# Optimization experiments

Measured on AMD Instinct MI355X. Metric: run time of the kernel, lower is better.

The kernel has to match this reference:

```python
import jax, jax.numpy as jnp
import numpy as np

TEMPERATURE = 0.2
EPS = 1e-12  # F.normalize clamp eps


def setup_inputs() -> dict:
    key = jax.random.key(0)
    k1, k2 = jax.random.split(key)
    N, D = 4096, 256
    Z_1 = jax.random.normal(k1, (N, D), dtype=jnp.float32)
    Z_2 = jax.random.normal(k2, (N, D), dtype=jnp.float32)
    return {"Z_1": Z_1, "Z_2": Z_2}


def reference(Z_1, Z_2):
    N = Z_1.shape[0]
    M = 2 * N
    # concat views and L2-normalize rows (torch F.normalize semantics)
    Z = jnp.concatenate([Z_1, Z_2], axis=0)  # [2N, D]
    Z = Z / jnp.maximum(jnp.linalg.norm(Z, axis=1, keepdims=True), EPS)
    # full similarity matrix [2N, 2N]
    sim = jnp.matmul(Z, Z.T) / TEMPERATURE
    # positive for row i is column (i + N) mod 2N (other view of same sample,
    # identity diagonal discarded as in create_contrastive_masks)
    idx = jnp.arange(M)
    pos = sim[idx, (idx + N) % M]  # [2N]
    # logits = [pos, negatives]; label = 0 => CE = logsumexp(pos U negs) - pos.
    # pos U negs = all columns except the identity diagonal.
    diag = idx[:, None] == idx[None, :]
    sim_masked = jnp.where(diag, -jnp.inf, sim)
    lse = jax.nn.logsumexp(sim_masked, axis=1)  # [2N]
    return jnp.mean(lse - pos)
```

## Files before the change

kernel.cpp:

```cpp
#include <hip/hip_runtime.h>
#include <cstdint>
#include <cstddef>

#define TINV 5.0f
#define C5L2E 7.2134752044448170f
#define NROWS 4096
#define DDIM 256
#define MM 8192

typedef __bf16 bf16x8 __attribute__((ext_vector_type(8)));
typedef float f32x4 __attribute__((ext_vector_type(4)));

typedef const void __attribute__((address_space(1)))* gas_ptr;
typedef void __attribute__((address_space(3)))* las_ptr;

__global__ __launch_bounds__(256, 2)
void nrm_kernel(const float* __restrict__ Z1, const float* __restrict__ Z2,
                unsigned short* __restrict__ Zb, float* __restrict__ rowsumAcc) {
    if (blockIdx.x < 32) rowsumAcc[blockIdx.x * 256 + threadIdx.x] = 0.f;
    const int w = threadIdx.x >> 6, lane = threadIdx.x & 63;
    const int row = blockIdx.x * 4 + w;
    const float* src = row < NROWS ? Z1 + (size_t)row * DDIM
                                   : Z2 + (size_t)(row - NROWS) * DDIM;
    float4 v = reinterpret_cast<const float4*>(src)[lane];
    float ss = v.x*v.x + v.y*v.y + v.z*v.z + v.w*v.w;
    #pragma unroll
    for (int m = 1; m < 64; m <<= 1) ss += __shfl_xor(ss, m, 64);
    float inv = 1.0f / fmaxf(sqrtf(ss), 1e-12f);
    float o[4] = { v.x*inv, v.y*inv, v.z*inv, v.w*inv };
    unsigned short us[4];
    #pragma unroll
    for (int e = 0; e < 4; ++e) {
        unsigned int b = __builtin_bit_cast(unsigned int, o[e]);
        b += 0x7FFFu + ((b >> 16) & 1u);
        us[e] = (unsigned short)(b >> 16);
    }
    reinterpret_cast<ushort4*>(Zb + (size_t)row * DDIM)[lane] =
        *reinterpret_cast<ushort4*>(us);
}

__device__ __forceinline__ void stage32(const unsigned short* Zb, char* ldsdst,
                                        int rowStart, int tid) {
    const char* base = reinterpret_cast<const char*>(Zb) + (size_t)rowStart * 512;
    #pragma unroll
    for (int it = 0; it < 8; ++it) {
        int L = it * 4096 + tid * 16;
        int row = L >> 9;
        int soff = row * 512 + ((L & 511) ^ ((row & 15) << 4));
        __builtin_amdgcn_global_load_lds((gas_ptr)(base + soff), (las_ptr)(ldsdst + L),
                                         16, 0, 0);
    }
}

__global__ __launch_bounds__(256, 2)
void sim_lse_kernel(const unsigned short* __restrict__ Zb,
                    float* __restrict__ rowsumAcc,
                    float* __restrict__ posArr) {
    __shared__ char lds[65536];
    __shared__ float colRed[4][128];
    const int tid = threadIdx.x;
    const int lane = tid & 63;
    const int w = tid >> 6;
    const int r15 = lane & 15, hi = lane >> 4;
    const int r = blockIdx.x >> 3;
    const int s = blockIdx.x & 7;
    const int e0 = r & 7, e1 = e0 ^ 4;
    const int nt = 8 + ((s == e0) || (s == e1));
    const int extraHalf = (s == e1) ? 1 : 0;
    const int R0 = r * 128;

    int koff[8];
    #pragma unroll
    for (int kk = 0; kk < 8; ++kk)
        koff[kk] = ((hi << 4) | (kk << 6)) ^ (r15 << 4);

    stage32(Zb, lds, R0, tid);
    stage32(Zb, lds + 32768, R0 + 64, tid);
    __syncthreads();
    bf16x8 qf[2][8];
    {
        const char* ab = lds + ((w >> 1) << 15);
        #pragma unroll
        for (int mf = 0; mf < 2; ++mf)
            #pragma unroll
            for (int kk = 0; kk < 8; ++kk)
                qf[mf][kk] = *reinterpret_cast<const bf16x8*>(
                    ab + ((w & 1) * 32 + mf * 16 + r15) * 512 + koff[kk]);
    }
    __syncthreads();

    int baddr[8];
    #pragma unroll
    for (int kk = 0; kk < 8; ++kk) baddr[kk] = r15 * 512 + koff[kk];

    float rowsum[2][4] = {{0,0,0,0},{0,0,0,0}};
    const int iBase = R0 + w * 32 + (hi << 2);

    auto colOf = [&](int t) -> int {
        int d = (t < 8) ? (s + ((t >> 1) << 3)) : 32;
        int half = (t < 8) ? (t & 1) : extraHalf;
        return ((r + d) & 63) * 128 + half * 64;
    };

    stage32(Zb, lds, colOf(0), tid);

    for (int t = 0; t < nt; ++t) {
        const int C0 = colOf(t);
        const int cur = (t & 1) << 15;
        if (t < nt - 1) {
            stage32(Zb, lds + (cur ^ 32768), colOf(t + 1), tid);
            asm volatile("s_waitcnt vmcnt(8)" ::: "memory");
        } else {
            asm volatile("s_waitcnt vmcnt(0)" ::: "memory");
        }
        __builtin_amdgcn_s_barrier();
        __builtin_amdgcn_sched_barrier(0);

        const int mode = (t == 8) ? 2 : ((s == 0 && t < 2) ? 1 : 0);
        #pragma unroll
        for (int nf = 0; nf < 4; ++nf) {
            f32x4 acc0 = {0,0,0,0}, acc1 = {0,0,0,0};
            #pragma unroll
            for (int kk = 0; kk < 8; ++kk) {
                bf16x8 b = *reinterpret_cast<const bf16x8*>(lds + cur + nf * 8192 + baddr[kk]);
                acc0 = __builtin_amdgcn_mfma_f32_16x16x32_bf16(qf[0][kk], b, acc0, 0, 0, 0);
                acc1 = __builtin_amdgcn_mfma_f32_16x16x32_bf16(qf[1][kk], b, acc1, 0, 0, 0);
            }
            const int j = C0 + nf * 16 + r15;
            if (mode == 0) {
                float s8 = 0.f;
                #pragma unroll
                for (int mf = 0; mf < 2; ++mf) {
                    const f32x4 a = mf ? acc1 : acc0;
                    #pragma unroll
                    for (int rr = 0; rr < 4; ++rr) {
                        float e = __builtin_amdgcn_exp2f(fmaf(a[rr], C5L2E, -C5L2E));
                        rowsum[mf][rr] += e;
                        s8 += e;
                    }
                }
                s8 += __shfl_xor(s8, 16, 64);
                s8 += __shfl_xor(s8, 32, 64);
                if (hi == 0) colRed[w][(t & 1) * 64 + nf * 16 + r15] = s8;
            } else if (mode == 1) {
                #pragma unroll
                for (int mf = 0; mf < 2; ++mf) {
                    const f32x4 a = mf ? acc1 : acc0;
                    #pragma unroll
                    for (int rr = 0; rr < 4; ++rr) {
                        const int i = iBase + mf * 16 + rr;
                        if (j != i)
                            rowsum[mf][rr] += __builtin_amdgcn_exp2f(fmaf(a[rr], C5L2E, -C5L2E));
                    }
                }
            } else {
                #pragma unroll
                for (int mf = 0; mf < 2; ++mf) {
                    const f32x4 a = mf ? acc1 : acc0;
                    #pragma unroll
                    for (int rr = 0; rr < 4; ++rr) {
                        const int i = iBase + mf * 16 + rr;
                        rowsum[mf][rr] += __builtin_amdgcn_exp2f(fmaf(a[rr], C5L2E, -C5L2E));
                        if (j == (i ^ 4096)) posArr[i] = a[rr] * TINV;
                    }
                }
            }
        }
        asm volatile("" ::: "memory");
        __builtin_amdgcn_sched_barrier(0);
        __builtin_amdgcn_s_barrier();

        if ((t & 1) == 1 && !(s == 0 && t == 1)) {
            if (tid < 128) {
                float v = colRed[0][tid] + colRed[1][tid] + colRed[2][tid] + colRed[3][tid];
                const int cc = ((r + s + ((t >> 1) << 3)) & 63) * 128;
                atomicAdd(&rowsumAcc[cc + tid], v);
            }
        }
    }

    #pragma unroll
    for (int mf = 0; mf < 2; ++mf)
        #pragma unroll
        for (int rr = 0; rr < 4; ++rr) {
            float v = rowsum[mf][rr];
            v += __shfl_xor(v, 1, 64);
            v += __shfl_xor(v, 2, 64);
            v += __shfl_xor(v, 4, 64);
            v += __shfl_xor(v, 8, 64);
            if (r15 == 0) atomicAdd(&rowsumAcc[iBase + mf * 16 + rr], v);
        }
}

__global__ __launch_bounds__(128)
void fin1_kernel(const float* __restrict__ rowsumAcc, const float* __restrict__ posArr,
                 float* __restrict__ blockSums) {
    const int tid = threadIdx.x;
    const int i = blockIdx.x * 128 + tid;
    double v = (double)(logf(rowsumAcc[i]) + 5.0f - posArr[i]);
    #pragma unroll
    for (int m = 1; m < 64; m <<= 1) v += __shfl_xor(v, m, 64);
    __shared__ double red[2];
    if ((tid & 63) == 0) red[tid >> 6] = v;
    __syncthreads();
    if (tid == 0) blockSums[blockIdx.x] = (float)(red[0] + red[1]);
}

__global__ __launch_bounds__(64)
void fin2_kernel(const float* __restrict__ blockSums, float* __restrict__ out) {
    double v = (double)blockSums[threadIdx.x];
    #pragma unroll
    for (int m = 1; m < 64; m <<= 1) v += __shfl_xor(v, m, 64);
    if (threadIdx.x == 0) out[0] = (float)(v / (double)MM);
}

extern "C" void kernel_launch(void* const* d_in, const int* in_sizes, int n_in,
                              void* d_out, int out_size, void* d_ws, size_t ws_size,
                              hipStream_t stream) {
    const float* Z1 = (const float*)d_in[0];
    const float* Z2 = (const float*)d_in[1];
    float* out = (float*)d_out;
    char* ws = (char*)d_ws;
    unsigned short* Zb = (unsigned short*)ws;
    float* posArr = (float*)(ws + (size_t)MM * DDIM * 2);
    float* rowsumAcc = (float*)(ws + (size_t)MM * DDIM * 2 + MM * 4);
    float* blockSums = (float*)(ws + (size_t)MM * DDIM * 2 + 2 * MM * 4);

    nrm_kernel<<<MM / 4, 256, 0, stream>>>(Z1, Z2, Zb, rowsumAcc);
    sim_lse_kernel<<<64 * 8, 256, 0, stream>>>(Zb, rowsumAcc, posArr);
    fin1_kernel<<<64, 128, 0, stream>>>(rowsumAcc, posArr, blockSums);
    fin2_kernel<<<1, 64, 0, stream>>>(blockSums, out);
}
```

Baseline: 44.52 us.

## Enlarge sim tile to 256 rows with 8 waves and AGPR-held query fragments

Reworks the symmetric similarity/LSE kernel to process 256-row blocks with 512 threads (8 waves in a 4x2 layout), halving the grid to 256 blocks. Query fragments are loaded straight from global memory into AGPRs and fed to inline-asm MFMA, and each B fragment loaded from LDS is reused across four row tiles. The aim is to cut LDS traffic and global staging per FLOP through more reuse. The column schedule is re-derived for 32 row blocks so the diagonal and positive tiles are still covered. Costs are higher register pressure and fewer, larger blocks that may leave CUs underfilled on a 256-CU device.

```diff
diff --git a/kernel.cpp b/kernel.cpp
--- a/kernel.cpp
+++ b/kernel.cpp
@@ -9,6 +9,7 @@
 #define MM 8192
 
 typedef __bf16 bf16x8 __attribute__((ext_vector_type(8)));
+typedef int i32x4 __attribute__((ext_vector_type(4)));
 typedef float f32x4 __attribute__((ext_vector_type(4)));
 
 typedef const void __attribute__((address_space(1)))* gas_ptr;
@@ -43,8 +44,8 @@
                                         int rowStart, int tid) {
     const char* base = reinterpret_cast<const char*>(Zb) + (size_t)rowStart * 512;
     #pragma unroll
-    for (int it = 0; it < 8; ++it) {
-        int L = it * 4096 + tid * 16;
+    for (int it = 0; it < 4; ++it) {
+        int L = it * 8192 + tid * 16;
         int row = L >> 9;
         int soff = row * 512 + ((L & 511) ^ ((row & 15) << 4));
         __builtin_amdgcn_global_load_lds((gas_ptr)(base + soff), (las_ptr)(ldsdst + L),
@@ -52,135 +53,121 @@
     }
 }
 
-__global__ __launch_bounds__(256, 2)
+__global__ __launch_bounds__(512, 2)
 void sim_lse_kernel(const unsigned short* __restrict__ Zb,
                     float* __restrict__ rowsumAcc,
                     float* __restrict__ posArr) {
     __shared__ char lds[65536];
-    __shared__ float colRed[4][128];
+    __shared__ float colRed[4][64];
     const int tid = threadIdx.x;
     const int lane = tid & 63;
     const int w = tid >> 6;
+    const int wr = w >> 1, wc = w & 1;
     const int r15 = lane & 15, hi = lane >> 4;
     const int r = blockIdx.x >> 3;
     const int s = blockIdx.x & 7;
-    const int e0 = r & 7, e1 = e0 ^ 4;
-    const int nt = 8 + ((s == e0) || (s == e1));
-    const int extraHalf = (s == e1) ? 1 : 0;
-    const int R0 = r * 128;
-
-    int koff[8];
-    #pragma unroll
-    for (int kk = 0; kk < 8; ++kk)
-        koff[kk] = ((hi << 4) | (kk << 6)) ^ (r15 << 4);
-
-    stage32(Zb, lds, R0, tid);
-    stage32(Zb, lds + 32768, R0 + 64, tid);
-    __syncthreads();
-    bf16x8 qf[2][8];
+    const int R0 = r * 256;
+    const int nt = (s < 4) ? 9 : 8;
+
+    auto colOf = [&](int t) -> int {
+        int d, q;
+        if (t == 8)        { d = 16;                  q = s; }
+        else if (s == 7)   { if (t < 4) { d = 8; q = t; } else { d = 0; q = t - 4; } }
+        else               { d = (t < 4) ? s + 1 : s + 9; q = t & 3; }
+        return ((r + d) & 31) * 256 + q * 64;
+    };
+
+    stage32(Zb, lds, colOf(0), tid);
+
+    i32x4 qf[4][8];
     {
-        const char* ab = lds + ((w >> 1) << 15);
+        const char* abase = reinterpret_cast<const char*>(Zb)
+                          + (size_t)(R0 + wr * 64 + r15) * 512 + hi * 16;
         #pragma unroll
-        for (int mf = 0; mf < 2; ++mf)
+        for (int mf = 0; mf < 4; ++mf)
             #pragma unroll
             for (int kk = 0; kk < 8; ++kk)
-                qf[mf][kk] = *reinterpret_cast<const bf16x8*>(
-                    ab + ((w & 1) * 32 + mf * 16 + r15) * 512 + koff[kk]);
-    }
-    __syncthreads();
-
-    int baddr[8];
-    #pragma unroll
-    for (int kk = 0; kk < 8; ++kk) baddr[kk] = r15 * 512 + koff[kk];
-
-    float rowsum[2][4] = {{0,0,0,0},{0,0,0,0}};
-    const int iBase = R0 + w * 32 + (hi << 2);
-
-    auto colOf = [&](int t) -> int {
-        int d = (t < 8) ? (s + ((t >> 1) << 3)) : 32;
-        int half = (t < 8) ? (t & 1) : extraHalf;
-        return ((r + d) & 63) * 128 + half * 64;
-    };
-
-    stage32(Zb, lds, colOf(0), tid);
+                qf[mf][kk] = *reinterpret_cast<const i32x4*>(abase + mf * 8192 + kk * 64);
+    }
+
+    int baddr0[8];
+    #pragma unroll
+    for (int kk = 0; kk < 8; ++kk)
+        baddr0[kk] = (wc * 32 + r15) * 512 + (((hi << 4) | (kk << 6)) ^ (r15 << 4));
+
+    float rowsum[4][4] = {{0,0,0,0},{0,0,0,0},{0,0,0,0},{0,0,0,0}};
+    const int iBase = R0 + wr * 64 + (hi << 2);
 
     for (int t = 0; t < nt; ++t) {
         const int C0 = colOf(t);
         const int cur = (t & 1) << 15;
         if (t < nt - 1) {
             stage32(Zb, lds + (cur ^ 32768), colOf(t + 1), tid);
-            asm volatile("s_waitcnt vmcnt(8)" ::: "memory");
+            asm volatile("s_waitcnt vmcnt(4)" ::: "memory");
         } else {
             asm volatile("s_waitcnt vmcnt(0)" ::: "memory");
         }
         __builtin_amdgcn_s_barrier();
         __builtin_amdgcn_sched_barrier(0);
 
-        const int mode = (t == 8) ? 2 : ((s == 0 && t < 2) ? 1 : 0);
+        const int mode = (t == 8) ? 2 : ((s == 7 && t >= 4) ? 1 : 0);
         #pragma unroll
-        for (int nf = 0; nf < 4; ++nf) {
-            f32x4 acc0 = {0,0,0,0}, acc1 = {0,0,0,0};
+        for (int nf = 0; nf < 2; ++nf) {
+            f32x4 acc[4] = {{0,0,0,0},{0,0,0,0},{0,0,0,0},{0,0,0,0}};
             #pragma unroll
             for (int kk = 0; kk < 8; ++kk) {
-                bf16x8 b = *reinterpret_cast<const bf16x8*>(lds + cur + nf * 8192 + baddr[kk]);
-                acc0 = __builtin_amdgcn_mfma_f32_16x16x32_bf16(qf[0][kk], b, acc0, 0, 0, 0);
-                acc1 = __builtin_amdgcn_mfma_f32_16x16x32_bf16(qf[1][kk], b, acc1, 0, 0, 0);
+                i32x4 b = *reinterpret_cast<const i32x4*>(lds + cur + nf * 8192 + baddr0[kk]);
+                #pragma unroll
+                for (int mf = 0; mf < 4; ++mf)
+                    asm("v_mfma_f32_16x16x32_bf16 %0, %1, %2, %0"
+                        : "+v"(acc[mf]) : "a"(qf[mf][kk]), "v"(b));
             }
-            const int j = C0 + nf * 16 + r15;
+            const int j = C0 + wc * 32 + nf * 16 + r15;
             if (mode == 0) {
                 float s8 = 0.f;
                 #pragma unroll
-                for (int mf = 0; mf < 2; ++mf) {
-                    const f32x4 a = mf ? acc1 : acc0;
+                for (int mf = 0; mf < 4; ++mf)
                     #pragma unroll
                     for (int rr = 0; rr < 4; ++rr) {
-                        float e = __builtin_amdgcn_exp2f(fmaf(a[rr], C5L2E, -C5L2E));
+                        float e = __builtin_amdgcn_exp2f(fmaf(acc[mf][rr], C5L2E, -C5L2E));
                         rowsum[mf][rr] += e;
                         s8 += e;
                     }
-                }
                 s8 += __shfl_xor(s8, 16, 64);
                 s8 += __shfl_xor(s8, 32, 64);
-                if (hi == 0) colRed[w][(t & 1) * 64 + nf * 16 + r15] = s8;
+                if (hi == 0) colRed[wr][wc * 32 + nf * 16 + r15] = s8;
             } else if (mode == 1) {
                 #pragma unroll
-                for (int mf = 0; mf < 2; ++mf) {
-                    const f32x4 a = mf ? acc1 : acc0;
+                for (int mf = 0; mf < 4; ++mf)
                     #pragma unroll
                     for (int rr = 0; rr < 4; ++rr) {
                         const int i = iBase + mf * 16 + rr;
                         if (j != i)
-                            rowsum[mf][rr] += __builtin_amdgcn_exp2f(fmaf(a[rr], C5L2E, -C5L2E));
+                            rowsum[mf][rr] += __builtin_amdgcn_exp2f(fmaf(acc[mf][rr], C5L2E, -C5L2E));
                     }
-                }
             } else {
                 #pragma unroll
-                for (int mf = 0; mf < 2; ++mf) {
-                    const f32x4 a = mf ? acc1 : acc0;
+                for (int mf = 0; mf < 4; ++mf)
                     #pragma unroll
                     for (int rr = 0; rr < 4; ++rr) {
                         const int i = iBase + mf * 16 + rr;
-                        rowsum[mf][rr] += __builtin_amdgcn_exp2f(fmaf(a[rr], C5L2E, -C5L2E));
-                        if (j == (i ^ 4096)) posArr[i] = a[rr] * TINV;
+                        rowsum[mf][rr] += __builtin_amdgcn_exp2f(fmaf(acc[mf][rr], C5L2E, -C5L2E));
+                        if (j == (i ^ 4096)) posArr[i] = acc[mf][rr] * TINV;
                     }
-                }
             }
         }
-        asm volatile("" ::: "memory");
+        asm volatile("s_waitcnt lgkmcnt(0)" ::: "memory");
         __builtin_amdgcn_sched_barrier(0);
         __builtin_amdgcn_s_barrier();
 
-        if ((t & 1) == 1 && !(s == 0 && t == 1)) {
-            if (tid < 128) {
-                float v = colRed[0][tid] + colRed[1][tid] + colRed[2][tid] + colRed[3][tid];
-                const int cc = ((r + s + ((t >> 1) << 3)) & 63) * 128;
-                atomicAdd(&rowsumAcc[cc + tid], v);
-            }
-        }
-    }
-
-    #pragma unroll
-    for (int mf = 0; mf < 2; ++mf)
+        if (mode == 0 && tid < 64) {
+            float v = colRed[0][tid] + colRed[1][tid] + colRed[2][tid] + colRed[3][tid];
+            atomicAdd(&rowsumAcc[C0 + tid], v);
+        }
+    }
+
+    #pragma unroll
+    for (int mf = 0; mf < 4; ++mf)
         #pragma unroll
         for (int rr = 0; rr < 4; ++rr) {
             float v = rowsum[mf][rr];
@@ -227,7 +214,7 @@
     float* blockSums = (float*)(ws + (size_t)MM * DDIM * 2 + 2 * MM * 4);
 
     nrm_kernel<<<MM / 4, 256, 0, stream>>>(Z1, Z2, Zb, rowsumAcc);
-    sim_lse_kernel<<<64 * 8, 256, 0, stream>>>(Zb, rowsumAcc, posArr);
+    sim_lse_kernel<<<32 * 8, 512, 0, stream>>>(Zb, rowsumAcc, posArr);
     fin1_kernel<<<64, 128, 0, stream>>>(rowsumAcc, posArr, blockSums);
     fin2_kernel<<<1, 64, 0, stream>>>(blockSums, out);
 }
```

After: 46.28 us. +4.0%, slower.

## Split sim work into 16 column slices with 32-column tiles and smaller LDS

Applied to the files above, without the earlier changes.

Doubles the grid to 1024 blocks by giving each block 16 column slices instead of 8, halving column tiles to 32 rows so LDS drops to 32KB and occupancy can rise to 4 blocks per CU. Query fragments are now loaded straight from global memory into registers instead of going through LDS, which removes the initial staging and two barriers. Column sums are atomically added every tile rather than every other tile, so there are more but smaller atomics and more barrier rounds per unit of work.

```diff
diff --git a/kernel.cpp b/kernel.cpp
--- a/kernel.cpp
+++ b/kernel.cpp
@@ -39,11 +39,11 @@
         *reinterpret_cast<ushort4*>(us);
 }
 
-__device__ __forceinline__ void stage32(const unsigned short* Zb, char* ldsdst,
+__device__ __forceinline__ void stage16(const unsigned short* Zb, char* ldsdst,
                                         int rowStart, int tid) {
     const char* base = reinterpret_cast<const char*>(Zb) + (size_t)rowStart * 512;
     #pragma unroll
-    for (int it = 0; it < 8; ++it) {
+    for (int it = 0; it < 4; ++it) {
         int L = it * 4096 + tid * 16;
         int row = L >> 9;
         int soff = row * 512 + ((L & 511) ^ ((row & 15) << 4));
@@ -52,77 +52,71 @@
     }
 }
 
-__global__ __launch_bounds__(256, 2)
+__global__ __launch_bounds__(256, 4)
 void sim_lse_kernel(const unsigned short* __restrict__ Zb,
                     float* __restrict__ rowsumAcc,
                     float* __restrict__ posArr) {
-    __shared__ char lds[65536];
-    __shared__ float colRed[4][128];
+    __shared__ char lds[32768];
+    __shared__ float colRed[4][32];
     const int tid = threadIdx.x;
     const int lane = tid & 63;
     const int w = tid >> 6;
     const int r15 = lane & 15, hi = lane >> 4;
-    const int r = blockIdx.x >> 3;
-    const int s = blockIdx.x & 7;
-    const int e0 = r & 7, e1 = e0 ^ 4;
-    const int nt = 8 + ((s == e0) || (s == e1));
-    const int extraHalf = (s == e1) ? 1 : 0;
+    const int r = blockIdx.x >> 4;
+    const int s = blockIdx.x & 15;
     const int R0 = r * 128;
-
-    int koff[8];
-    #pragma unroll
-    for (int kk = 0; kk < 8; ++kk)
-        koff[kk] = ((hi << 4) | (kk << 6)) ^ (r15 << 4);
-
-    stage32(Zb, lds, R0, tid);
-    stage32(Zb, lds + 32768, R0 + 64, tid);
-    __syncthreads();
+    const bool hasExtra = (s & 3) == (r & 3);
+    const int q32 = s >> 2;
+    const int nt = hasExtra ? 9 : 8;
+
+    auto colOf = [&](int t) -> int {
+        if (t == 8) return ((r + 32) & 63) * 128 + q32 * 32;
+        int d = (t < 4) ? s : s + 16;
+        return ((r + d) & 63) * 128 + (t & 3) * 32;
+    };
+
+    stage16(Zb, lds, colOf(0), tid);
+
     bf16x8 qf[2][8];
     {
-        const char* ab = lds + ((w >> 1) << 15);
+        const char* abase = reinterpret_cast<const char*>(Zb)
+                          + (size_t)(R0 + w * 32 + r15) * 512 + hi * 16;
         #pragma unroll
         for (int mf = 0; mf < 2; ++mf)
             #pragma unroll
             for (int kk = 0; kk < 8; ++kk)
-                qf[mf][kk] = *reinterpret_cast<const bf16x8*>(
-                    ab + ((w & 1) * 32 + mf * 16 + r15) * 512 + koff[kk]);
-    }
-    __syncthreads();
+                qf[mf][kk] = *reinterpret_cast<const bf16x8*>(abase + mf * 8192 + kk * 64);
+    }
 
     int baddr[8];
     #pragma unroll
-    for (int kk = 0; kk < 8; ++kk) baddr[kk] = r15 * 512 + koff[kk];
+    for (int kk = 0; kk < 8; ++kk)
+        baddr[kk] = r15 * 512 + (((hi << 4) | (kk << 6)) ^ (r15 << 4));
 
     float rowsum[2][4] = {{0,0,0,0},{0,0,0,0}};
     const int iBase = R0 + w * 32 + (hi << 2);
 
-    auto colOf = [&](int t) -> int {
-        int d = (t < 8) ? (s + ((t >> 1) << 3)) : 32;
-        int half = (t < 8) ? (t & 1) : extraHalf;
-        return ((r + d) & 63) * 128 + half * 64;
-    };
-
-    stage32(Zb, lds, colOf(0), tid);
-
     for (int t = 0; t < nt; ++t) {
         const int C0 = colOf(t);
-        const int cur = (t & 1) << 15;
+        char* curb = lds + ((t & 1) << 14);
+        const bool pf = (t > 0) && !(s == 0 && t < 5) && (t != 9);
         if (t < nt - 1) {
-            stage32(Zb, lds + (cur ^ 32768), colOf(t + 1), tid);
-            asm volatile("s_waitcnt vmcnt(8)" ::: "memory");
+            stage16(Zb, lds + (((t & 1) ^ 1) << 14), colOf(t + 1), tid);
+            if (pf) asm volatile("s_waitcnt vmcnt(5)" ::: "memory");
+            else    asm volatile("s_waitcnt vmcnt(4)" ::: "memory");
         } else {
             asm volatile("s_waitcnt vmcnt(0)" ::: "memory");
         }
         __builtin_amdgcn_s_barrier();
         __builtin_amdgcn_sched_barrier(0);
 
-        const int mode = (t == 8) ? 2 : ((s == 0 && t < 2) ? 1 : 0);
+        const int mode = (t == 8) ? 2 : ((s == 0 && t < 4) ? 1 : 0);
         #pragma unroll
-        for (int nf = 0; nf < 4; ++nf) {
+        for (int nf = 0; nf < 2; ++nf) {
             f32x4 acc0 = {0,0,0,0}, acc1 = {0,0,0,0};
             #pragma unroll
             for (int kk = 0; kk < 8; ++kk) {
-                bf16x8 b = *reinterpret_cast<const bf16x8*>(lds + cur + nf * 8192 + baddr[kk]);
+                bf16x8 b = *reinterpret_cast<const bf16x8*>(curb + nf * 8192 + baddr[kk]);
                 acc0 = __builtin_amdgcn_mfma_f32_16x16x32_bf16(qf[0][kk], b, acc0, 0, 0, 0);
                 acc1 = __builtin_amdgcn_mfma_f32_16x16x32_bf16(qf[1][kk], b, acc1, 0, 0, 0);
             }
@@ -141,7 +135,7 @@
                 }
                 s8 += __shfl_xor(s8, 16, 64);
                 s8 += __shfl_xor(s8, 32, 64);
-                if (hi == 0) colRed[w][(t & 1) * 64 + nf * 16 + r15] = s8;
+                if (hi == 0) colRed[w][nf * 16 + r15] = s8;
             } else if (mode == 1) {
                 #pragma unroll
                 for (int mf = 0; mf < 2; ++mf) {
@@ -166,16 +160,13 @@
                 }
             }
         }
-        asm volatile("" ::: "memory");
+        asm volatile("s_waitcnt lgkmcnt(0)" ::: "memory");
         __builtin_amdgcn_sched_barrier(0);
         __builtin_amdgcn_s_barrier();
 
-        if ((t & 1) == 1 && !(s == 0 && t == 1)) {
-            if (tid < 128) {
-                float v = colRed[0][tid] + colRed[1][tid] + colRed[2][tid] + colRed[3][tid];
-                const int cc = ((r + s + ((t >> 1) << 3)) & 63) * 128;
-                atomicAdd(&rowsumAcc[cc + tid], v);
-            }
+        if (mode == 0 && tid < 32) {
+            float v = colRed[0][tid] + colRed[1][tid] + colRed[2][tid] + colRed[3][tid];
+            atomicAdd(&rowsumAcc[C0 + tid], v);
         }
     }
 
@@ -222,12 +213,12 @@
     float* out = (float*)d_out;
     char* ws = (char*)d_ws;
     unsigned short* Zb = (unsigned short*)ws;
-    float* posArr = (float*)(ws + (size_t)MM * DDIM * 2);
-    float* rowsumAcc = (float*)(ws + (size_t)MM * DDIM * 2 + MM * 4);
-    float* blockSums = (float*)(ws + (size_t)MM * DDIM * 2 + 2 * MM * 4);
+    float* posArr = (float*)(ws + 4194304);
+    float* rowsumAcc = (float*)(ws + 4194304 + 32768);
+    float* blockSums = (float*)(ws + 4194304 + 65536);
 
     nrm_kernel<<<MM / 4, 256, 0, stream>>>(Z1, Z2, Zb, rowsumAcc);
-    sim_lse_kernel<<<64 * 8, 256, 0, stream>>>(Zb, rowsumAcc, posArr);
+    sim_lse_kernel<<<64 * 16, 256, 0, stream>>>(Zb, rowsumAcc, posArr);
     fin1_kernel<<<64, 128, 0, stream>>>(rowsumAcc, posArr, blockSums);
     fin2_kernel<<<1, 64, 0, stream>>>(blockSums, out);
 }
```

Result: slower. 46.03 us (+3.4%).
